# Optimization experiments

Measured on AMD Instinct MI355X. Metric: run time of the kernel, lower is better.

The kernel has to match this reference:

```python
import jax, jax.numpy as jnp
import numpy as np

N, M, D = 4096, 4096, 8

def laplace_tensor_markov(x, grid, lengthscale):
    # product over dims of exp(-|x_i - y_j|/ls) == exp(-sum_d |x_id - y_jd|/ls_d)
    # x: [n,d], grid: [m,d] -> [n,m]
    diff = jnp.abs(x[:, None, :] - grid[None, :, :]) / lengthscale  # [n,m,d]
    return jnp.exp(-jnp.sum(diff, axis=-1))

def setup_inputs() -> dict:
    key = jax.random.key(0)
    k1, k2, k3 = jax.random.split(key, 3)
    x = jax.random.normal(k1, (N, D), dtype=jnp.float32)
    sparse_grid = jax.random.uniform(k2, (M, D), dtype=jnp.float32)
    # inverse Cholesky factor is lower-triangular; emulate its structured sparsity
    L = jax.random.normal(k3, (M, M), dtype=jnp.float32) * 0.02
    chol_inv = jnp.tril(L) + jnp.eye(M, dtype=jnp.float32)
    lengthscale = jnp.ones((D,), dtype=jnp.float32)
    return {"x": x, "sparse_grid": sparse_grid, "chol_inv": chol_inv, "lengthscale": lengthscale}

def reference(x, sparse_grid, chol_inv, lengthscale):
    k_star = laplace_tensor_markov(x, sparse_grid, lengthscale)  # [n,m]
    phi = k_star @ chol_inv                                      # [n,m]
    return phi
```

## Files before the change

### kernel.cpp

```cpp
#include <hip/hip_runtime.h>
#include <cstdint>
#include <cstddef>

typedef unsigned short u16;
typedef __bf16 bf16x8 __attribute__((ext_vector_type(8)));
typedef float floatx4 __attribute__((ext_vector_type(4)));

#define NPTS 4096
#define MGRD 4096
#define DDIM 8

static __device__ __forceinline__ u16 f2bf(float f) {
    uint32_t u = __float_as_uint(f);
    u += 0x7fffu + ((u >> 16) & 1u);
    return (u16)(u >> 16);
}

__global__ __launch_bounds__(256) void prep_kernel(
    const float* __restrict__ x, const float* __restrict__ g,
    const float* __restrict__ ls, const float* __restrict__ B,
    u16* __restrict__ A, u16* __restrict__ Bt)
{
    __shared__ float tile[64][65];
    const int bid = blockIdx.x;
    const int tid = threadIdx.x;

    if (bid < 512) {
        const int kb = bid & 1;
        const int n0 = (bid >> 1) * 16;
        const int k0 = kb * 2048 + tid * 8;

        float il[DDIM];
#pragma unroll
        for (int d = 0; d < DDIM; ++d) il[d] = 1.0f / ls[d];

        float4 g0[8], g1[8];
#pragma unroll
        for (int r = 0; r < 8; ++r) {
            g0[r] = *reinterpret_cast<const float4*>(g + (size_t)(k0 + r) * DDIM);
            g1[r] = *reinterpret_cast<const float4*>(g + (size_t)(k0 + r) * DDIM + 4);
        }

        for (int nn = 0; nn < 16; ++nn) {
            const int n = n0 + nn;
            const float4 x0 = *reinterpret_cast<const float4*>(x + (size_t)n * DDIM);
            const float4 x1 = *reinterpret_cast<const float4*>(x + (size_t)n * DDIM + 4);
            alignas(16) u16 res[8];
#pragma unroll
            for (int r = 0; r < 8; ++r) {
                float s = fabsf(x0.x - g0[r].x) * il[0] + fabsf(x0.y - g0[r].y) * il[1]
                        + fabsf(x0.z - g0[r].z) * il[2] + fabsf(x0.w - g0[r].w) * il[3]
                        + fabsf(x1.x - g1[r].x) * il[4] + fabsf(x1.y - g1[r].y) * il[5]
                        + fabsf(x1.z - g1[r].z) * il[6] + fabsf(x1.w - g1[r].w) * il[7];
                res[r] = f2bf(__expf(-s));
            }
            *reinterpret_cast<uint4*>(A + (size_t)n * MGRD + k0) =
                *reinterpret_cast<const uint4*>(res);
        }
    } else {
        const int id = bid - 512;
        const int bx = id & 63;
        const int by = id >> 6;
        if (by < (bx & ~1)) return;
        const int k0 = by * 64;
        const int m0 = bx * 64;

#pragma unroll
        for (int r = 0; r < 4; ++r) {
            int c   = r * 256 + tid;
            int row = c >> 4;
            int col = (c & 15) * 4;
            const float4 v = *reinterpret_cast<const float4*>(&B[(size_t)(k0 + row) * MGRD + m0 + col]);
            tile[row][col + 0] = v.x; tile[row][col + 1] = v.y;
            tile[row][col + 2] = v.z; tile[row][col + 3] = v.w;
        }
        __syncthreads();

#pragma unroll
        for (int r = 0; r < 2; ++r) {
            int c  = r * 256 + tid;
            int mr = c >> 3;
            int kc = (c & 7) * 8;
            alignas(16) u16 tmp[8];
#pragma unroll
            for (int j = 0; j < 8; ++j)
                tmp[j] = f2bf(tile[kc + j][mr]);
            *reinterpret_cast<uint4*>(&Bt[(size_t)(m0 + mr) * MGRD + k0 + kc]) =
                *reinterpret_cast<const uint4*>(tmp);
        }
    }
}

__global__ __launch_bounds__(256, 3) void gemm_bt_kernel(
    const u16* __restrict__ A,
    const u16* __restrict__ Bt,
    float* __restrict__ C)
{
    __shared__ u16 sA[128 * 64] __attribute__((aligned(16)));
    __shared__ u16 sB[128 * 64] __attribute__((aligned(16)));

    const int tid   = threadIdx.x;
    const int lane  = tid & 63;
    const int w     = tid >> 6;
    const int wbase = w * 64;
    const int wm    = (w >> 1) * 64;
    const int wn    = (w & 1) * 64;

    const int l  = blockIdx.x;
    const int t  = l >> 8;
    const int r_ = l & 255;
    const int b  = r_ & 31;
    const int bm = (t & 1) ? (31 - b) : b;
    const int bn = (r_ >> 5) + 8 * t;
    const int bn0 = bn * 128;
    const int bm0 = bm * 128;

    const int lrow  = lane & 15;
    const int lhi   = lane >> 4;
    const int r7    = lrow & 7;

    floatx4 acc[4][4];
#pragma unroll
    for (int i = 0; i < 4; ++i)
#pragma unroll
        for (int j = 0; j < 4; ++j)
            acc[i][j] = (floatx4)0.0f;

    for (int k0 = 4096 - 64; k0 >= bm0; k0 -= 64) {
#pragma unroll
        for (int r = 0; r < 4; ++r) {
            int c   = r * 256 + tid;
            int row = c >> 3;
            int kc  = ((c ^ (c >> 3)) & 7) * 8;
            const u16* ga = A  + (size_t)(bn0 + row) * 4096 + k0 + kc;
            const u16* gb = Bt + (size_t)(bm0 + row) * 4096 + k0 + kc;
            __builtin_amdgcn_global_load_lds(
                (const __attribute__((address_space(1))) void*)ga,
                (__attribute__((address_space(3))) void*)(sA + (size_t)(r * 256 + wbase) * 8),
                16, 0, 0);
            __builtin_amdgcn_global_load_lds(
                (const __attribute__((address_space(1))) void*)gb,
                (__attribute__((address_space(3))) void*)(sB + (size_t)(r * 256 + wbase) * 8),
                16, 0, 0);
        }
        __syncthreads();

#pragma unroll
        for (int s = 0; s < 2; ++s) {
            const int sw = ((s * 4 + lhi) ^ r7) * 8;
            bf16x8 af[4], bfr[4];
#pragma unroll
            for (int i = 0; i < 4; ++i)
                af[i] = *reinterpret_cast<const bf16x8*>(
                    &sA[(size_t)(wm + i * 16 + lrow) * 64 + sw]);
#pragma unroll
            for (int j = 0; j < 4; ++j)
                bfr[j] = *reinterpret_cast<const bf16x8*>(
                    &sB[(size_t)(wn + j * 16 + lrow) * 64 + sw]);
#pragma unroll
            for (int i = 0; i < 4; ++i)
#pragma unroll
                for (int j = 0; j < 4; ++j)
                    acc[i][j] = __builtin_amdgcn_mfma_f32_16x16x32_bf16(
                        af[i], bfr[j], acc[i][j], 0, 0, 0);
        }
        __syncthreads();
    }

#pragma unroll
    for (int i = 0; i < 4; ++i) {
        int rown = bn0 + wm + i * 16 + lhi * 4;
#pragma unroll
        for (int j = 0; j < 4; ++j) {
            int colm = bm0 + wn + j * 16 + lrow;
            float* cp = C + (size_t)rown * 4096 + colm;
#pragma unroll
            for (int rr = 0; rr < 4; ++rr)
                cp[(size_t)rr * 4096] = acc[i][j][rr];
        }
    }
}

extern "C" void kernel_launch(void* const* d_in, const int* in_sizes, int n_in,
                              void* d_out, int out_size, void* d_ws, size_t ws_size,
                              hipStream_t stream)
{
    const float* x    = (const float*)d_in[0];
    const float* grid = (const float*)d_in[1];
    const float* ci   = (const float*)d_in[2];
    const float* ls   = (const float*)d_in[3];
    float* out = (float*)d_out;

    u16* wsA  = (u16*)d_ws;
    u16* wsBt = (u16*)d_ws + (size_t)MGRD * MGRD;

    prep_kernel<<<dim3(512 + 64 * 64), 256, 0, stream>>>(x, grid, ls, ci, wsA, wsBt);
    gemm_bt_kernel<<<dim3(1024), 256, 0, stream>>>(wsA, wsBt, out);
}
```

Before: 201.0 us.

## Replace GEMM with 8-wave 256x128 tile kernel using split-buffer staged pipeline

Swaps the 256-thread 128x128 GEMM for a 512-thread kernel with a 256x128 output tile. A and B tiles are split into halves that are loaded asynchronously into LDS and interleaved with quadrant-wise MFMA groups, using explicit vmcnt waits, barriers and setprio. The goal is to overlap global-to-LDS loads with matrix math and to raise reuse per loaded tile, while keeping the triangular k-range skip. The cost is more complex hand-scheduled synchronisation, fewer blocks for load balancing across the triangular work, and a risk of race or ordering bugs.

```diff
diff --git a/kernel.cpp b/kernel.cpp
--- a/kernel.cpp
+++ b/kernel.cpp
@@ -91,33 +91,73 @@
     }
 }
 
-__global__ __launch_bounds__(256, 3) void gemm_bt_kernel(
+
+#define FENCE() asm volatile("" ::: "memory")
+static __device__ __forceinline__ void bar() {
+    FENCE(); __builtin_amdgcn_s_barrier(); FENCE();
+}
+
+__global__ __launch_bounds__(512, 2) void gemm8_kernel(
     const u16* __restrict__ A,
     const u16* __restrict__ Bt,
     float* __restrict__ C)
 {
-    __shared__ u16 sA[128 * 64] __attribute__((aligned(16)));
-    __shared__ u16 sB[128 * 64] __attribute__((aligned(16)));
-
-    const int tid   = threadIdx.x;
-    const int lane  = tid & 63;
-    const int w     = tid >> 6;
-    const int wbase = w * 64;
-    const int wm    = (w >> 1) * 64;
-    const int wn    = (w & 1) * 64;
-
-    const int l  = blockIdx.x;
-    const int t  = l >> 8;
-    const int r_ = l & 255;
-    const int b  = r_ & 31;
-    const int bm = (t & 1) ? (31 - b) : b;
-    const int bn = (r_ >> 5) + 8 * t;
-    const int bn0 = bn * 128;
-    const int bm0 = bm * 128;
-
-    const int lrow  = lane & 15;
-    const int lhi   = lane >> 4;
-    const int r7    = lrow & 7;
+    __shared__ u16 sA[2][128 * 64] __attribute__((aligned(16)));
+    __shared__ u16 sB[2][64 * 64]  __attribute__((aligned(16)));
+
+    const int tid  = threadIdx.x;
+    const int lane = tid & 63;
+    const int w    = tid >> 6;
+    const int wn   = (w >> 1) * 64;
+    const int wmm  = (w & 1) * 64;
+    const int lrow = lane & 15;
+    const int lhi  = lane >> 4;
+    const int r7   = lrow & 7;
+
+    const int id  = blockIdx.x;
+    const int bm  = id >> 4;
+    const int bn  = id & 15;
+    const int bn0 = bn << 8;
+    const int bm0 = bm << 7;
+    const int L   = 64 - 2 * bm;
+
+    int aoff[2][2], boff[2];
+#pragma unroll
+    for (int h = 0; h < 2; ++h)
+#pragma unroll
+        for (int r = 0; r < 2; ++r) {
+            int c    = r * 512 + tid;
+            int rowh = c >> 3;
+            int kc   = ((c ^ rowh) & 7) * 8;
+            int grow = bn0 + (rowh >> 5) * 64 + h * 32 + (rowh & 31);
+            aoff[h][r] = grow * 4096 + kc;
+        }
+#pragma unroll
+    for (int h = 0; h < 2; ++h) {
+        int rowh = tid >> 3;
+        int kc   = ((tid ^ rowh) & 7) * 8;
+        int growm = bm0 + (rowh >> 5) * 64 + h * 32 + (rowh & 31);
+        boff[h] = growm * 4096 + kc;
+    }
+
+#define STAGE_A(h, r, k)                                                        \
+    __builtin_amdgcn_global_load_lds(                                           \
+        (const __attribute__((address_space(1))) void*)(A + (size_t)aoff[h][r] + (k)), \
+        (__attribute__((address_space(3))) void*)(&sA[h][((r) * 512 + w * 64) * 8]),   \
+        16, 0, 0)
+#define STAGE_B(h, k)                                                           \
+    __builtin_amdgcn_global_load_lds(                                           \
+        (const __attribute__((address_space(1))) void*)(Bt + (size_t)boff[h] + (k)),   \
+        (__attribute__((address_space(3))) void*)(&sB[h][(w * 64) * 8]),        \
+        16, 0, 0)
+
+    const int aidx0 = wn >> 1;
+    const int bidx0 = wmm >> 1;
+
+#define RD_A(i, s) (*reinterpret_cast<const bf16x8*>(                           \
+    &sA[(i) >> 1][(size_t)(aidx0 + ((i) & 1) * 16 + lrow) * 64 + ((((s) * 4 + lhi) ^ r7) * 8)]))
+#define RD_B(j, s) (*reinterpret_cast<const bf16x8*>(                           \
+    &sB[(j) >> 1][(size_t)(bidx0 + ((j) & 1) * 16 + lrow) * 64 + ((((s) * 4 + lhi) ^ r7) * 8)]))
 
     floatx4 acc[4][4];
 #pragma unroll
@@ -126,53 +166,80 @@
         for (int j = 0; j < 4; ++j)
             acc[i][j] = (floatx4)0.0f;
 
-    for (int k0 = 4096 - 64; k0 >= bm0; k0 -= 64) {
-#pragma unroll
-        for (int r = 0; r < 4; ++r) {
-            int c   = r * 256 + tid;
-            int row = c >> 3;
-            int kc  = ((c ^ (c >> 3)) & 7) * 8;
-            const u16* ga = A  + (size_t)(bn0 + row) * 4096 + k0 + kc;
-            const u16* gb = Bt + (size_t)(bm0 + row) * 4096 + k0 + kc;
-            __builtin_amdgcn_global_load_lds(
-                (const __attribute__((address_space(1))) void*)ga,
-                (__attribute__((address_space(3))) void*)(sA + (size_t)(r * 256 + wbase) * 8),
-                16, 0, 0);
-            __builtin_amdgcn_global_load_lds(
-                (const __attribute__((address_space(1))) void*)gb,
-                (__attribute__((address_space(3))) void*)(sB + (size_t)(r * 256 + wbase) * 8),
-                16, 0, 0);
-        }
-        __syncthreads();
-
-#pragma unroll
-        for (int s = 0; s < 2; ++s) {
-            const int sw = ((s * 4 + lhi) ^ r7) * 8;
-            bf16x8 af[4], bfr[4];
-#pragma unroll
-            for (int i = 0; i < 4; ++i)
-                af[i] = *reinterpret_cast<const bf16x8*>(
-                    &sA[(size_t)(wm + i * 16 + lrow) * 64 + sw]);
-#pragma unroll
-            for (int j = 0; j < 4; ++j)
-                bfr[j] = *reinterpret_cast<const bf16x8*>(
-                    &sB[(size_t)(wn + j * 16 + lrow) * 64 + sw]);
-#pragma unroll
-            for (int i = 0; i < 4; ++i)
-#pragma unroll
-                for (int j = 0; j < 4; ++j)
-                    acc[i][j] = __builtin_amdgcn_mfma_f32_16x16x32_bf16(
-                        af[i], bfr[j], acc[i][j], 0, 0, 0);
-        }
-        __syncthreads();
-    }
+    bf16x8 af[4][2], bfr[4][2];
+
+#define READ_AF01() do { af[0][0]=RD_A(0,0); af[0][1]=RD_A(0,1);                \
+                         af[1][0]=RD_A(1,0); af[1][1]=RD_A(1,1); } while (0)
+#define READ_AF23() do { af[2][0]=RD_A(2,0); af[2][1]=RD_A(2,1);                \
+                         af[3][0]=RD_A(3,0); af[3][1]=RD_A(3,1); } while (0)
+#define READ_BF01() do { bfr[0][0]=RD_B(0,0); bfr[0][1]=RD_B(0,1);              \
+                         bfr[1][0]=RD_B(1,0); bfr[1][1]=RD_B(1,1); } while (0)
+#define READ_BF23() do { bfr[2][0]=RD_B(2,0); bfr[2][1]=RD_B(2,1);              \
+                         bfr[3][0]=RD_B(3,0); bfr[3][1]=RD_B(3,1); } while (0)
+
+#define MM(i, j, s) acc[i][j] = __builtin_amdgcn_mfma_f32_16x16x32_bf16(        \
+    af[i][s], bfr[j][s], acc[i][j], 0, 0, 0)
+#define MFMA_Q(qi, qj) do {                                                     \
+    __builtin_amdgcn_s_setprio(1);                                              \
+    MM(2*(qi)+0, 2*(qj)+0, 0); MM(2*(qi)+0, 2*(qj)+1, 0);                       \
+    MM(2*(qi)+1, 2*(qj)+0, 0); MM(2*(qi)+1, 2*(qj)+1, 0);                       \
+    MM(2*(qi)+0, 2*(qj)+0, 1); MM(2*(qi)+0, 2*(qj)+1, 1);                       \
+    MM(2*(qi)+1, 2*(qj)+0, 1); MM(2*(qi)+1, 2*(qj)+1, 1);                       \
+    __builtin_amdgcn_s_setprio(0);                                              \
+} while (0)
+
+    int kT = 4096 - 64;
+    STAGE_A(0, 0, kT); STAGE_A(0, 1, kT);
+    STAGE_B(0, kT);
+    STAGE_B(1, kT);
+    STAGE_A(1, 0, kT); STAGE_A(1, 1, kT);
+    asm volatile("s_waitcnt vmcnt(3)" ::: "memory");
+    bar();
+
+    for (int T = 0; T < L - 1; ++T, kT -= 64) {
+        const int kn = kT - 64;
+        READ_AF01(); READ_BF01();
+        bar();
+        MFMA_Q(0, 0);
+        asm volatile("s_waitcnt vmcnt(2)" ::: "memory");
+        bar();
+        READ_BF23();
+        STAGE_A(0, 0, kn); STAGE_A(0, 1, kn); STAGE_B(0, kn);
+        bar();
+        MFMA_Q(0, 1);
+        asm volatile("s_waitcnt vmcnt(3)" ::: "memory");
+        bar();
+        READ_AF23();
+        STAGE_B(1, kn);
+        bar();
+        MFMA_Q(1, 0);
+        bar();
+        STAGE_A(1, 0, kn); STAGE_A(1, 1, kn);
+        bar();
+        MFMA_Q(1, 1);
+        asm volatile("s_waitcnt vmcnt(3)" ::: "memory");
+        bar();
+    }
+
+    READ_AF01(); READ_BF01();
+    bar();
+    MFMA_Q(0, 0);
+    asm volatile("s_waitcnt vmcnt(2)" ::: "memory");
+    bar();
+    READ_BF23();
+    MFMA_Q(0, 1);
+    asm volatile("s_waitcnt vmcnt(0)" ::: "memory");
+    bar();
+    READ_AF23();
+    MFMA_Q(1, 0);
+    MFMA_Q(1, 1);
 
 #pragma unroll
     for (int i = 0; i < 4; ++i) {
-        int rown = bn0 + wm + i * 16 + lhi * 4;
+        int rown = bn0 + wn + i * 16 + lhi * 4;
 #pragma unroll
         for (int j = 0; j < 4; ++j) {
-            int colm = bm0 + wn + j * 16 + lrow;
+            int colm = bm0 + wmm + j * 16 + lrow;
             float* cp = C + (size_t)rown * 4096 + colm;
 #pragma unroll
             for (int rr = 0; rr < 4; ++rr)
@@ -195,5 +262,5 @@
     u16* wsBt = (u16*)d_ws + (size_t)MGRD * MGRD;
 
     prep_kernel<<<dim3(512 + 64 * 64), 256, 0, stream>>>(x, grid, ls, ci, wsA, wsBt);
-    gemm_bt_kernel<<<dim3(1024), 256, 0, stream>>>(wsA, wsBt, out);
-}
+    gemm8_kernel<<<dim3(512), 512, 0, stream>>>(wsA, wsBt, out);
+}
```

Result: no change. 197.9 us (-1.6%).

## Rewrite GEMM with 256x128 tiles, split-K wave groups and triple-buffered LDS pipeline

Applied to the files above, without the earlier changes.

Replaces the 128x128 single-buffered GEMM with a 512-thread kernel using 256x128 output tiles. Two wave groups each handle half of every 64-wide K slab and their partial sums are reduced through LDS at the end. Global-to-LDS loads are issued two stages ahead through a 3-slot ring, and MFMA bursts are interleaved with raised wave priority. The aim is to hide memory latency and raise arithmetic intensity, at the cost of more LDS use, a final reduction step, and less even per-block work on the triangular K range, since block count drops to 512.

```diff
diff --git a/kernel.cpp b/kernel.cpp
--- a/kernel.cpp
+++ b/kernel.cpp
@@ -91,92 +91,192 @@
     }
 }
 
-__global__ __launch_bounds__(256, 3) void gemm_bt_kernel(
+
+#define FENCE() asm volatile("" ::: "memory")
+static __device__ __forceinline__ void bar() {
+    FENCE(); __builtin_amdgcn_s_barrier(); FENCE();
+}
+
+__global__ __launch_bounds__(512, 2) void gemm_kh_kernel(
     const u16* __restrict__ A,
     const u16* __restrict__ Bt,
     float* __restrict__ C)
 {
-    __shared__ u16 sA[128 * 64] __attribute__((aligned(16)));
-    __shared__ u16 sB[128 * 64] __attribute__((aligned(16)));
-
-    const int tid   = threadIdx.x;
-    const int lane  = tid & 63;
-    const int w     = tid >> 6;
-    const int wbase = w * 64;
-    const int wm    = (w >> 1) * 64;
-    const int wn    = (w & 1) * 64;
-
-    const int l  = blockIdx.x;
-    const int t  = l >> 8;
-    const int r_ = l & 255;
-    const int b  = r_ & 31;
-    const int bm = (t & 1) ? (31 - b) : b;
-    const int bn = (r_ >> 5) + 8 * t;
-    const int bn0 = bn * 128;
-    const int bm0 = bm * 128;
-
-    const int lrow  = lane & 15;
-    const int lhi   = lane >> 4;
-    const int r7    = lrow & 7;
-
-    floatx4 acc[4][4];
-#pragma unroll
-    for (int i = 0; i < 4; ++i)
+    __shared__ u16 lds[3 * 24576] __attribute__((aligned(16)));
+
+    const int tid  = threadIdx.x;
+    const int lane = tid & 63;
+    const int w    = tid >> 6;
+    const int kg   = w >> 2;
+    const int wq   = w & 3;
+    const int nq   = wq >> 1;
+    const int mq   = wq & 1;
+    const int lrow = lane & 15;
+    const int lhi  = lane >> 4;
+    const int r7   = lrow & 7;
+
+    const int id  = blockIdx.x;
+    const int bm  = id >> 4;
+    const int bn  = id & 15;
+    const int bn0 = bn << 8;
+    const int bm0 = bm << 7;
+    const int L   = 64 - 2 * bm;
+
+    const int arow = tid >> 3;
+    const int aswz = ((tid ^ arow) & 7) * 8;
+    int aoff[4], boff[2];
+#pragma unroll
+    for (int r = 0; r < 4; ++r)
+        aoff[r] = (bn0 + r * 64 + arow) * 4096 + aswz;
+#pragma unroll
+    for (int r = 0; r < 2; ++r)
+        boff[r] = (bm0 + r * 64 + arow) * 4096 + aswz;
+
+    const int ldst = w * 512;
+    const int cswz = ((kg * 4 + lhi) ^ r7) * 8;
+    const int rowA = (nq * 128 + lrow) * 64 + cswz;
+    const int rowB = (mq * 64  + lrow) * 64 + cswz;
+
+#define STG_A(QA, R, K) __builtin_amdgcn_global_load_lds(                        \
+    (const __attribute__((address_space(1))) void*)(A + (size_t)aoff[R] + (K)),  \
+    (__attribute__((address_space(3))) void*)((QA) + (R) * 4096 + ldst), 16, 0, 0)
+#define STG_B(QB, R, K) __builtin_amdgcn_global_load_lds(                        \
+    (const __attribute__((address_space(1))) void*)(Bt + (size_t)boff[R] + (K)), \
+    (__attribute__((address_space(3))) void*)((QB) + (R) * 4096 + ldst), 16, 0, 0)
+
+    bf16x8 af[4], bfv[4];
+
+#define RDA(PA, IB) do {                                                         \
+    af[0] = *reinterpret_cast<const bf16x8*>((PA) + rowA + ((IB) + 0) * 1024);   \
+    af[1] = *reinterpret_cast<const bf16x8*>((PA) + rowA + ((IB) + 1) * 1024);   \
+    af[2] = *reinterpret_cast<const bf16x8*>((PA) + rowA + ((IB) + 2) * 1024);   \
+    af[3] = *reinterpret_cast<const bf16x8*>((PA) + rowA + ((IB) + 3) * 1024);   \
+} while (0)
+#define RDB(PB) do {                                                             \
+    bfv[0] = *reinterpret_cast<const bf16x8*>((PB) + rowB + 0 * 1024);           \
+    bfv[1] = *reinterpret_cast<const bf16x8*>((PB) + rowB + 1 * 1024);           \
+    bfv[2] = *reinterpret_cast<const bf16x8*>((PB) + rowB + 2 * 1024);           \
+    bfv[3] = *reinterpret_cast<const bf16x8*>((PB) + rowB + 3 * 1024);           \
+} while (0)
+
+    floatx4 acc[8][4];
+#pragma unroll
+    for (int i = 0; i < 8; ++i)
 #pragma unroll
         for (int j = 0; j < 4; ++j)
             acc[i][j] = (floatx4)0.0f;
 
-    for (int k0 = 4096 - 64; k0 >= bm0; k0 -= 64) {
-#pragma unroll
-        for (int r = 0; r < 4; ++r) {
-            int c   = r * 256 + tid;
-            int row = c >> 3;
-            int kc  = ((c ^ (c >> 3)) & 7) * 8;
-            const u16* ga = A  + (size_t)(bn0 + row) * 4096 + k0 + kc;
-            const u16* gb = Bt + (size_t)(bm0 + row) * 4096 + k0 + kc;
-            __builtin_amdgcn_global_load_lds(
-                (const __attribute__((address_space(1))) void*)ga,
-                (__attribute__((address_space(3))) void*)(sA + (size_t)(r * 256 + wbase) * 8),
-                16, 0, 0);
-            __builtin_amdgcn_global_load_lds(
-                (const __attribute__((address_space(1))) void*)gb,
-                (__attribute__((address_space(3))) void*)(sB + (size_t)(r * 256 + wbase) * 8),
-                16, 0, 0);
-        }
-        __syncthreads();
-
-#pragma unroll
-        for (int s = 0; s < 2; ++s) {
-            const int sw = ((s * 4 + lhi) ^ r7) * 8;
-            bf16x8 af[4], bfr[4];
-#pragma unroll
-            for (int i = 0; i < 4; ++i)
-                af[i] = *reinterpret_cast<const bf16x8*>(
-                    &sA[(size_t)(wm + i * 16 + lrow) * 64 + sw]);
+#define MF(a, b, c) __builtin_amdgcn_mfma_f32_16x16x32_bf16(a, b, c, 0, 0, 0)
+#define MFMA16(IB) do {                                                          \
+    __builtin_amdgcn_s_setprio(1);                                               \
+    acc[(IB)+0][0] = MF(af[0], bfv[0], acc[(IB)+0][0]);                          \
+    acc[(IB)+0][1] = MF(af[0], bfv[1], acc[(IB)+0][1]);                          \
+    acc[(IB)+0][2] = MF(af[0], bfv[2], acc[(IB)+0][2]);                          \
+    acc[(IB)+0][3] = MF(af[0], bfv[3], acc[(IB)+0][3]);                          \
+    acc[(IB)+1][0] = MF(af[1], bfv[0], acc[(IB)+1][0]);                          \
+    acc[(IB)+1][1] = MF(af[1], bfv[1], acc[(IB)+1][1]);                          \
+    acc[(IB)+1][2] = MF(af[1], bfv[2], acc[(IB)+1][2]);                          \
+    acc[(IB)+1][3] = MF(af[1], bfv[3], acc[(IB)+1][3]);                          \
+    acc[(IB)+2][0] = MF(af[2], bfv[0], acc[(IB)+2][0]);                          \
+    acc[(IB)+2][1] = MF(af[2], bfv[1], acc[(IB)+2][1]);                          \
+    acc[(IB)+2][2] = MF(af[2], bfv[2], acc[(IB)+2][2]);                          \
+    acc[(IB)+2][3] = MF(af[2], bfv[3], acc[(IB)+2][3]);                          \
+    acc[(IB)+3][0] = MF(af[3], bfv[0], acc[(IB)+3][0]);                          \
+    acc[(IB)+3][1] = MF(af[3], bfv[1], acc[(IB)+3][1]);                          \
+    acc[(IB)+3][2] = MF(af[3], bfv[2], acc[(IB)+3][2]);                          \
+    acc[(IB)+3][3] = MF(af[3], bfv[3], acc[(IB)+3][3]);                          \
+    __builtin_amdgcn_s_setprio(0);                                               \
+} while (0)
+
+    int kT = 4096 - 64;
+    {
+        u16* qA0 = lds;                 u16* qB0 = lds + 16384;
+        u16* qA1 = lds + 24576;         u16* qB1 = lds + 24576 + 16384;
+        STG_A(qA0, 0, kT); STG_A(qA0, 1, kT); STG_A(qA0, 2, kT); STG_A(qA0, 3, kT);
+        STG_B(qB0, 0, kT); STG_B(qB0, 1, kT);
+        STG_A(qA1, 0, kT - 64); STG_A(qA1, 1, kT - 64);
+        STG_A(qA1, 2, kT - 64); STG_A(qA1, 3, kT - 64);
+        STG_B(qB1, 0, kT - 64); STG_B(qB1, 1, kT - 64);
+    }
+    asm volatile("s_waitcnt vmcnt(6)" ::: "memory");
+    bar();
+
+    int p = 0;
+    for (int T = 0; T < L - 2; ++T) {
+        u16* pA = lds + p * 24576;      u16* pB = pA + 16384;
+        int p2 = p + 2; if (p2 >= 3) p2 -= 3;
+        u16* qA = lds + p2 * 24576;     u16* qB = qA + 16384;
+        const int kst = kT - 128;
+
+        RDA(pA, 0); RDB(pB);
+        STG_A(qA, 0, kst); STG_A(qA, 1, kst); STG_B(qB, 0, kst);
+        bar();
+        MFMA16(0);
+        bar();
+        RDA(pA, 4);
+        STG_A(qA, 2, kst); STG_A(qA, 3, kst); STG_B(qB, 1, kst);
+        bar();
+        MFMA16(4);
+        asm volatile("s_waitcnt vmcnt(6)" ::: "memory");
+        bar();
+
+        kT -= 64; ++p; if (p == 3) p = 0;
+    }
+
+    {
+        u16* pA = lds + p * 24576;      u16* pB = pA + 16384;
+        RDA(pA, 0); RDB(pB);
+        bar();
+        MFMA16(0);
+        bar();
+        RDA(pA, 4);
+        bar();
+        MFMA16(4);
+        asm volatile("s_waitcnt vmcnt(0)" ::: "memory");
+        bar();
+        kT -= 64; ++p; if (p == 3) p = 0;
+    }
+    {
+        u16* pA = lds + p * 24576;      u16* pB = pA + 16384;
+        RDA(pA, 0); RDB(pB);
+        bar();
+        MFMA16(0);
+        bar();
+        RDA(pA, 4);
+        bar();
+        MFMA16(4);
+    }
+
+    __syncthreads();
+    float* scr = reinterpret_cast<float*>(lds);
+    if (kg == 1) {
+#pragma unroll
+        for (int i = 0; i < 8; ++i)
 #pragma unroll
             for (int j = 0; j < 4; ++j)
-                bfr[j] = *reinterpret_cast<const bf16x8*>(
-                    &sB[(size_t)(wn + j * 16 + lrow) * 64 + sw]);
-#pragma unroll
-            for (int i = 0; i < 4; ++i)
-#pragma unroll
-                for (int j = 0; j < 4; ++j)
-                    acc[i][j] = __builtin_amdgcn_mfma_f32_16x16x32_bf16(
-                        af[i], bfr[j], acc[i][j], 0, 0, 0);
-        }
-        __syncthreads();
-    }
-
-#pragma unroll
-    for (int i = 0; i < 4; ++i) {
-        int rown = bn0 + wm + i * 16 + lhi * 4;
-#pragma unroll
-        for (int j = 0; j < 4; ++j) {
-            int colm = bm0 + wn + j * 16 + lrow;
-            float* cp = C + (size_t)rown * 4096 + colm;
-#pragma unroll
-            for (int rr = 0; rr < 4; ++rr)
-                cp[(size_t)rr * 4096] = acc[i][j][rr];
+                *reinterpret_cast<floatx4*>(
+                    scr + (size_t)wq * 8192 + (i * 4 + j) * 256 + lane * 4) = acc[i][j];
+    }
+    __syncthreads();
+    if (kg == 0) {
+#pragma unroll
+        for (int i = 0; i < 8; ++i)
+#pragma unroll
+            for (int j = 0; j < 4; ++j)
+                acc[i][j] += *reinterpret_cast<const floatx4*>(
+                    scr + (size_t)wq * 8192 + (i * 4 + j) * 256 + lane * 4);
+
+#pragma unroll
+        for (int i = 0; i < 8; ++i) {
+            int rown = bn0 + nq * 128 + i * 16 + lhi * 4;
+#pragma unroll
+            for (int j = 0; j < 4; ++j) {
+                int colm = bm0 + mq * 64 + j * 16 + lrow;
+                float* cp = C + (size_t)rown * 4096 + colm;
+#pragma unroll
+                for (int rr = 0; rr < 4; ++rr)
+                    cp[(size_t)rr * 4096] = acc[i][j][rr];
+            }
         }
     }
 }
@@ -195,5 +295,5 @@
     u16* wsBt = (u16*)d_ws + (size_t)MGRD * MGRD;
 
     prep_kernel<<<dim3(512 + 64 * 64), 256, 0, stream>>>(x, grid, ls, ci, wsA, wsBt);
-    gemm_bt_kernel<<<dim3(1024), 256, 0, stream>>>(wsA, wsBt, out);
-}
+    gemm_kh_kernel<<<dim3(512), 512, 0, stream>>>(wsA, wsBt, out);
+}
```

After: 189.7 us. 1.06x faster.

## Replace GEMM with 256x256 tile, 8-phase pipelined kernel and split-K triangular balancing

Applied to the files above, without the earlier changes.

Replaces the 128x128 single-buffered GEMM with a 512-thread, 256x256-tile kernel that double-buffers LDS and interleaves global-to-LDS prefetch with MFMA phases under explicit waitcnt and barrier control. Triangular work is balanced by giving each of the 256 blocks one or two K-segments, with split-K partial results combined through atomic adds into an output that the prep kernel now zero-fills. The goal is more data reuse per tile, better load/compute overlap and even block loads. In exchange it adds atomics, an extra output-zeroing pass and a more fragile hand-tuned schedule.

```diff
diff --git a/kernel.cpp b/kernel.cpp
--- a/kernel.cpp
+++ b/kernel.cpp
@@ -9,6 +9,9 @@
 #define NPTS 4096
 #define MGRD 4096
 #define DDIM 8
+
+#define AS1 __attribute__((address_space(1)))
+#define AS3 __attribute__((address_space(3)))
 
 static __device__ __forceinline__ u16 f2bf(float f) {
     uint32_t u = __float_as_uint(f);
@@ -19,7 +22,7 @@
 __global__ __launch_bounds__(256) void prep_kernel(
     const float* __restrict__ x, const float* __restrict__ g,
     const float* __restrict__ ls, const float* __restrict__ B,
-    u16* __restrict__ A, u16* __restrict__ Bt)
+    u16* __restrict__ A, u16* __restrict__ Bt, float* __restrict__ C)
 {
     __shared__ float tile[64][65];
     const int bid = blockIdx.x;
@@ -57,11 +60,11 @@
             *reinterpret_cast<uint4*>(A + (size_t)n * MGRD + k0) =
                 *reinterpret_cast<const uint4*>(res);
         }
-    } else {
+    } else if (bid < 4608) {
         const int id = bid - 512;
         const int bx = id & 63;
         const int by = id >> 6;
-        if (by < (bx & ~1)) return;
+        if (by < (bx & ~3)) return;
         const int k0 = by * 64;
         const int m0 = bx * 64;
 
@@ -88,95 +91,179 @@
             *reinterpret_cast<uint4*>(&Bt[(size_t)(m0 + mr) * MGRD + k0 + kc]) =
                 *reinterpret_cast<const uint4*>(tmp);
         }
+    } else {
+        const int z   = bid - 4608;
+        const int row = z * 4 + (tid >> 6);
+        float4* cp = reinterpret_cast<float4*>(C + (size_t)row * MGRD);
+        const int cb = tid & 63;
+#pragma unroll
+        for (int v = 0; v < 8; ++v)
+            cp[cb + v * 64] = make_float4(0.f, 0.f, 0.f, 0.f);
     }
 }
 
-__global__ __launch_bounds__(256, 3) void gemm_bt_kernel(
+
+#define FENCE() asm volatile("" ::: "memory")
+static __device__ __forceinline__ void bar() {
+    FENCE(); __builtin_amdgcn_s_barrier(); FENCE();
+}
+#define LGKM0() do { asm volatile("s_waitcnt lgkmcnt(0)" ::: "memory");          \
+                     __builtin_amdgcn_sched_barrier(0); } while (0)
+#define VMCNT6() asm volatile("s_waitcnt vmcnt(6)" ::: "memory")
+#define VMCNT0() asm volatile("s_waitcnt vmcnt(0)" ::: "memory")
+
+__global__ __launch_bounds__(512, 2) void gemm_8ph_kernel(
     const u16* __restrict__ A,
     const u16* __restrict__ Bt,
     float* __restrict__ C)
 {
-    __shared__ u16 sA[128 * 64] __attribute__((aligned(16)));
-    __shared__ u16 sB[128 * 64] __attribute__((aligned(16)));
-
-    const int tid   = threadIdx.x;
-    const int lane  = tid & 63;
-    const int w     = tid >> 6;
-    const int wbase = w * 64;
-    const int wm    = (w >> 1) * 64;
-    const int wn    = (w & 1) * 64;
-
-    const int l  = blockIdx.x;
-    const int t  = l >> 8;
-    const int r_ = l & 255;
-    const int b  = r_ & 31;
-    const int bm = (t & 1) ? (31 - b) : b;
-    const int bn = (r_ >> 5) + 8 * t;
-    const int bn0 = bn * 128;
-    const int bm0 = bm * 128;
-
-    const int lrow  = lane & 15;
-    const int lhi   = lane >> 4;
-    const int r7    = lrow & 7;
-
-    floatx4 acc[4][4];
-#pragma unroll
-    for (int i = 0; i < 4; ++i)
-#pragma unroll
-        for (int j = 0; j < 4; ++j)
-            acc[i][j] = (floatx4)0.0f;
-
-    for (int k0 = 4096 - 64; k0 >= bm0; k0 -= 64) {
-#pragma unroll
-        for (int r = 0; r < 4; ++r) {
-            int c   = r * 256 + tid;
-            int row = c >> 3;
-            int kc  = ((c ^ (c >> 3)) & 7) * 8;
-            const u16* ga = A  + (size_t)(bn0 + row) * 4096 + k0 + kc;
-            const u16* gb = Bt + (size_t)(bm0 + row) * 4096 + k0 + kc;
-            __builtin_amdgcn_global_load_lds(
-                (const __attribute__((address_space(1))) void*)ga,
-                (__attribute__((address_space(3))) void*)(sA + (size_t)(r * 256 + wbase) * 8),
-                16, 0, 0);
-            __builtin_amdgcn_global_load_lds(
-                (const __attribute__((address_space(1))) void*)gb,
-                (__attribute__((address_space(3))) void*)(sB + (size_t)(r * 256 + wbase) * 8),
-                16, 0, 0);
-        }
-        __syncthreads();
-
-#pragma unroll
-        for (int s = 0; s < 2; ++s) {
-            const int sw = ((s * 4 + lhi) ^ r7) * 8;
-            bf16x8 af[4], bfr[4];
-#pragma unroll
-            for (int i = 0; i < 4; ++i)
-                af[i] = *reinterpret_cast<const bf16x8*>(
-                    &sA[(size_t)(wm + i * 16 + lrow) * 64 + sw]);
+    __shared__ u16 lds[2 * 32768] __attribute__((aligned(16)));
+
+    const int tid  = threadIdx.x;
+    const int lane = tid & 63;
+    const int w    = tid >> 6;
+    const int wm   = (w >> 2) * 128;
+    const int wn   = (w & 3) * 64;
+    const int lrow = lane & 15;
+    const int lhi  = lane >> 4;
+    const int r7   = lrow & 7;
+
+    const int id   = blockIdx.x;
+    const int bn   = id & 15;
+    const int slot = id >> 4;
+    const int bn0  = bn << 8;
+
+    const int arow  = tid >> 3;
+    const int aswz  = ((tid ^ arow) & 7) * 8;
+    const int aoffb = (bn0 + arow) * 4096 + aswz;
+    const int ldst  = w * 512;
+
+    const int c0    = (lhi ^ r7) * 8;
+    const int c1    = ((4 + lhi) ^ r7) * 8;
+    const int baseA = (wm + lrow) * 64;
+    const int baseB = 16384 + (wn + lrow) * 64;
+
+    int nseg, bm_0, lo_0, hi_0, bm_1, lo_1, hi_1;
+    if (slot < 8) {
+        nseg = 1; bm_0 = slot;  lo_0 = 32;            hi_0 = 64;
+        bm_1 = 0; lo_1 = 0; hi_1 = 0;
+    } else {
+        const int p = slot - 8;
+        nseg = 2; bm_0 = p;      lo_0 = 4 * p;        hi_0 = 32;
+                  bm_1 = 15 - p; lo_1 = 4 * (15 - p); hi_1 = 64;
+    }
+
+    floatx4 acc[8][4];
+    bf16x8 af[8][2], bv[4][2];
+
+#define STGA(D, R, T) __builtin_amdgcn_global_load_lds(                          \
+    (const AS1 void*)(A + (size_t)(aoffb + (R) * 262144 + ((lo + (T)) << 6))),   \
+    (AS3 void*)(lds + (D) * 32768 + (R) * 4096 + ldst), 16, 0, 0)
+#define STGB(D, R, T) __builtin_amdgcn_global_load_lds(                          \
+    (const AS1 void*)(Bt + (size_t)(boffb + (R) * 262144 + ((lo + (T)) << 6))),  \
+    (AS3 void*)(lds + (D) * 32768 + 16384 + (R) * 4096 + ldst), 16, 0, 0)
+
+#define RA(I, S, D) af[I][S] = *reinterpret_cast<const bf16x8*>(                 \
+    lds + (D) * 32768 + baseA + (I) * 1024 + ((S) ? c1 : c0))
+#define RB(J, S, D) bv[J][S] = *reinterpret_cast<const bf16x8*>(                 \
+    lds + (D) * 32768 + baseB + (J) * 1024 + ((S) ? c1 : c0))
+
+#define MQ(QI, QJ) do {                                                          \
+    __builtin_amdgcn_s_setprio(1);                                               \
+    _Pragma("unroll") for (int i_ = 0; i_ < 4; ++i_)                             \
+    _Pragma("unroll") for (int j_ = 0; j_ < 2; ++j_)                             \
+    _Pragma("unroll") for (int s_ = 0; s_ < 2; ++s_)                             \
+        acc[(QI) * 4 + i_][(QJ) * 2 + j_] =                                      \
+            __builtin_amdgcn_mfma_f32_16x16x32_bf16(                             \
+                af[(QI) * 4 + i_][s_], bv[(QJ) * 2 + j_][s_],                    \
+                acc[(QI) * 4 + i_][(QJ) * 2 + j_], 0, 0, 0);                     \
+    __builtin_amdgcn_s_setprio(0);                                               \
+} while (0)
+
+#define TILE(D, T) do {                                                          \
+                                              \
+    RA(0, 0, D); RA(0, 1, D); RA(1, 0, D); RA(1, 1, D);                          \
+    RA(2, 0, D); RA(2, 1, D); RA(3, 0, D); RA(3, 1, D);                          \
+    RB(0, 0, D); RB(0, 1, D); RB(1, 0, D); RB(1, 1, D);                          \
+    if ((T) + 1 < Ls) { STGA((D) ^ 1, 1, (T) + 1); STGA((D) ^ 1, 3, (T) + 1); }  \
+    bar(); LGKM0();                                                              \
+    MQ(0, 0);                                                                    \
+    bar();                                                                       \
+                                                            \
+    RB(2, 0, D); RB(2, 1, D); RB(3, 0, D); RB(3, 1, D);                          \
+    if ((T) + 2 < Ls) { STGA(D, 0, (T) + 2); STGA(D, 2, (T) + 2); }              \
+    bar(); LGKM0();                                                              \
+    MQ(0, 1);                                                                    \
+    bar();                                                                       \
+                                                            \
+    RA(4, 0, D); RA(4, 1, D); RA(5, 0, D); RA(5, 1, D);                          \
+    RA(6, 0, D); RA(6, 1, D); RA(7, 0, D); RA(7, 1, D);                          \
+    if ((T) + 2 < Ls) { STGB(D, 0, (T) + 2); STGB(D, 1, (T) + 2); }              \
+    bar(); LGKM0();                                                              \
+    MQ(1, 0);                                                                    \
+    bar();                                                                       \
+                                                               \
+    if ((T) + 2 < Ls) { STGB(D, 2, (T) + 2); STGB(D, 3, (T) + 2); }              \
+    bar();                                                                       \
+    MQ(1, 1);                                                                    \
+    if ((T) + 2 < Ls)      { VMCNT6(); }                                         \
+    else if ((T) + 1 < Ls) { VMCNT0(); }                                         \
+    bar();                                                                       \
+} while (0)
+
+    for (int sg = 0; sg < nseg; ++sg) {
+        int bm, lo, hi;
+        if (sg == 0) { bm = bm_0; lo = lo_0; hi = hi_0; }
+        else         { bm = bm_1; lo = lo_1; hi = hi_1; }
+        const int Ls  = hi - lo;
+        const int bm0 = bm << 8;
+        const int boffb = (bm0 + arow) * 4096 + aswz;
+
+#pragma unroll
+        for (int i = 0; i < 8; ++i)
 #pragma unroll
             for (int j = 0; j < 4; ++j)
-                bfr[j] = *reinterpret_cast<const bf16x8*>(
-                    &sB[(size_t)(wn + j * 16 + lrow) * 64 + sw]);
-#pragma unroll
-            for (int i = 0; i < 4; ++i)
-#pragma unroll
-                for (int j = 0; j < 4; ++j)
-                    acc[i][j] = __builtin_amdgcn_mfma_f32_16x16x32_bf16(
-                        af[i], bfr[j], acc[i][j], 0, 0, 0);
-        }
-        __syncthreads();
-    }
-
-#pragma unroll
-    for (int i = 0; i < 4; ++i) {
-        int rown = bn0 + wm + i * 16 + lhi * 4;
-#pragma unroll
-        for (int j = 0; j < 4; ++j) {
-            int colm = bm0 + wn + j * 16 + lrow;
-            float* cp = C + (size_t)rown * 4096 + colm;
-#pragma unroll
-            for (int rr = 0; rr < 4; ++rr)
-                cp[(size_t)rr * 4096] = acc[i][j][rr];
+                acc[i][j] = (floatx4)0.0f;
+
+        STGA(0, 0, 0); STGA(0, 2, 0);
+        STGB(0, 0, 0); STGB(0, 1, 0); STGB(0, 2, 0); STGB(0, 3, 0);
+        STGA(0, 1, 0); STGA(0, 3, 0);
+        STGA(1, 0, 1); STGA(1, 2, 1);
+        STGB(1, 0, 1); STGB(1, 1, 1); STGB(1, 2, 1); STGB(1, 3, 1);
+        VMCNT6();
+        bar();
+
+        for (int T = 0; T + 1 < Ls; T += 2) {
+            TILE(0, T);
+            TILE(1, T + 1);
+        }
+
+        if (bm < 8) {
+#pragma unroll
+            for (int i = 0; i < 8; ++i) {
+                const int rown = bn0 + wm + i * 16 + lhi * 4;
+#pragma unroll
+                for (int j = 0; j < 4; ++j) {
+                    const int colm = bm0 + wn + j * 16 + lrow;
+                    float* cp = C + (size_t)rown * 4096 + colm;
+#pragma unroll
+                    for (int rr = 0; rr < 4; ++rr)
+                        unsafeAtomicAdd(cp + (size_t)rr * 4096, acc[i][j][rr]);
+                }
+            }
+        } else {
+#pragma unroll
+            for (int i = 0; i < 8; ++i) {
+                const int rown = bn0 + wm + i * 16 + lhi * 4;
+#pragma unroll
+                for (int j = 0; j < 4; ++j) {
+                    const int colm = bm0 + wn + j * 16 + lrow;
+                    float* cp = C + (size_t)rown * 4096 + colm;
+#pragma unroll
+                    for (int rr = 0; rr < 4; ++rr)
+                        cp[(size_t)rr * 4096] = acc[i][j][rr];
+                }
+            }
         }
     }
 }
@@ -194,6 +281,6 @@
     u16* wsA  = (u16*)d_ws;
     u16* wsBt = (u16*)d_ws + (size_t)MGRD * MGRD;
 
-    prep_kernel<<<dim3(512 + 64 * 64), 256, 0, stream>>>(x, grid, ls, ci, wsA, wsBt);
-    gemm_bt_kernel<<<dim3(1024), 256, 0, stream>>>(wsA, wsBt, out);
-}
+    prep_kernel<<<dim3(512 + 4096 + 1024), 256, 0, stream>>>(x, grid, ls, ci, wsA, wsBt, out);
+    gemm_8ph_kernel<<<dim3(256), 512, 0, stream>>>(wsA, wsBt, out);
+}
```

Result: slower. 228.2 us (+13.5%).
